# Optimization experiments

Hardware: AMD Instinct MI355X
Metric: run time of the kernel (lower is better)

The kernel has to match this reference:

```python
import jax, jax.numpy as jnp
import numpy as np

# Straight-through sign binarization: forward -> {-1, +1}, backward -> identity
@jax.custom_vjp
def binarize(x):
    return jnp.where(x >= 0, jnp.ones_like(x), -jnp.ones_like(x))

def _bin_fwd(x):
    return binarize(x), None

def _bin_bwd(res, g):
    return (g,)

binarize.defvjp(_bin_fwd, _bin_bwd)

BATCH = 16384
IN_SIZE = 1025   # must be 2**n + 1
HIDDEN = 1025    # must be 2**n + 1

def setup_inputs() -> dict:
    key = jax.random.key(0)
    k0, k1, k2, k3 = jax.random.split(key, 4)
    # weight init scale per reset_parameters: sqrt(1.5/(in+out)) uniform
    s = float(np.sqrt(1.5 / (IN_SIZE + HIDDEN)))
    return {
        "x": jax.random.normal(k0, (BATCH, IN_SIZE), dtype=jnp.float32),
        "W0": jax.random.uniform(k1, (HIDDEN, IN_SIZE), jnp.float32, -s, s),
        "W1": jax.random.uniform(k2, (HIDDEN, HIDDEN), jnp.float32, -s, s),
        "W2": jax.random.uniform(k3, (1, HIDDEN), jnp.float32, -s, s),
    }

def reference(x, W0, W1, W2):
    # x: [B, IN_SIZE]; weights stored [out, in] (nn.Linear convention), no bias
    h = x.reshape(-1, IN_SIZE)
    for W in (W0, W1, W2):
        lin = h @ binarize(W).T          # float GEMM against +/-1 weights
        h = binarize(lin)                # sign activation
    # num_classes == 2 path: to_boolean maps {-1,+1} -> {0,1}, then squeeze
    out = (h + 1.0) * 0.5
    return out.squeeze(-1)               # [B]
```

## Files before the change

### kernel.cpp

```cpp
#include <hip/hip_runtime.h>
#include <cstdint>

typedef unsigned long long u64;
typedef unsigned short ushort_t;
typedef __attribute__((ext_vector_type(8))) short short8;
typedef __attribute__((ext_vector_type(4))) float f32x4;

#define B_TOTAL 16384
#define K_DIM   1025
#define O_DIM   1025
#define NWORDS  17
#define NKT     34
#define NFRAG   72
#define A_BYTES 8192
#define B_BYTES 73728
#define STEP_BYTES (A_BYTES + B_BYTES)
#define FLAG_CAP 4096
#define L23_ROWS 16

__device__ __forceinline__ ushort_t f2bf_rne(float f) {
  unsigned u = __float_as_uint(f);
  return (ushort_t)((u + 0x7fffu + ((u >> 16) & 1u)) >> 16);
}

__device__ __forceinline__ void gload16(const ushort_t* g, char* l) {
  __builtin_amdgcn_global_load_lds(
      (const __attribute__((address_space(1))) void*)g,
      (__attribute__((address_space(3))) void*)l, 16, 0, 0);
}

__global__ __launch_bounds__(256) void pack_all_kernel(const float* __restrict__ W0,
                                                       const float* __restrict__ W1,
                                                       const float* __restrict__ W2,
                                                       u64* __restrict__ w0b,
                                                       u64* __restrict__ w1b,
                                                       u64* __restrict__ w2b) {
  __shared__ unsigned char by[136];
  const int row = blockIdx.x, t = threadIdx.x;
  const float* src; u64* dst; int o;
  if (row < O_DIM)           { src = W0; dst = w0b; o = row; }
  else if (row < 2 * O_DIM)  { src = W1; dst = w1b; o = row - O_DIM; }
  else                       { src = W2; dst = w2b; o = 0; }
  if (t < 136) {
    const float* wr = src + (size_t)o * K_DIM;
    unsigned m = 0;
#pragma unroll
    for (int j = 0; j < 8; ++j) {
      int k = t * 8 + j;
      bool pos = (k < K_DIM) ? (wr[k] >= 0.0f) : true;
      m |= (unsigned)pos << j;
    }
    by[t] = (unsigned char)m;
  }
  __syncthreads();
  if (t < NWORDS) {
    u64 word = 0;
#pragma unroll
    for (int q = 0; q < 8; ++q) word |= (u64)by[t * 8 + q] << (8 * q);
    dst[(size_t)o * NWORDS + t] = word;
  }
}

__global__ __launch_bounds__(256) void prep_sbf_kernel(const float* __restrict__ w0,
                                                       ushort_t* __restrict__ sbf) {
  const int t = threadIdx.x;
  const int f = blockIdx.x * 4 + (t >> 6);
  const int lane = t & 63;
  const int kt = f / NFRAG, nf = f % NFRAG;
  const int o = nf * 16 + (lane & 15);
  const int kbase = kt * 32 + (lane >> 4) * 8;
  short8 sv;
#pragma unroll
  for (int j = 0; j < 8; ++j) {
    int k = kbase + j;
    short v = 0;
    if (o < O_DIM && k < K_DIM)
      v = (short)((w0[(size_t)o * K_DIM + k] >= 0.0f) ? 0x3F80 : 0xBF80);
    sv[j] = v;
  }
  *(short8*)&sbf[(size_t)f * 512 + lane * 8] = sv;
}

__global__ __launch_bounds__(256) void prep_xf_kernel(const float* __restrict__ x,
                                                      ushort_t* __restrict__ xf,
                                                      float* __restrict__ errb) {
  const int p = blockIdx.x, t = threadIdx.x;
  const int mf = t >> 6, lane = t & 63;
  const int lr = lane & 15, lg = lane >> 4;
  const int brow = p * 64 + mf * 16 + lr;
  const float* xr = x + (size_t)brow * K_DIM;
  float s = 0.0f;
  for (int kt = 0; kt < NKT; ++kt) {
    const int kbase = kt * 32 + lg * 8;
    float v[8];
    if (kbase + 8 <= K_DIM) {
      float4 a = *(const float4*)(xr + kbase);
      float4 b = *(const float4*)(xr + kbase + 4);
      v[0]=a.x; v[1]=a.y; v[2]=a.z; v[3]=a.w; v[4]=b.x; v[5]=b.y; v[6]=b.z; v[7]=b.w;
    } else {
#pragma unroll
      for (int j = 0; j < 8; ++j) v[j] = (kbase + j < K_DIM) ? xr[kbase + j] : 0.0f;
    }
    short8 hi, lo;
#pragma unroll
    for (int j = 0; j < 8; ++j) {
      s += fabsf(v[j]);
      ushort_t h = f2bf_rne(v[j]);
      float hf = __uint_as_float((unsigned)h << 16);
      ushort_t l = f2bf_rne(v[j] - hf);
      hi[j] = (short)h; lo[j] = (short)l;
    }
    size_t base = ((size_t)(p * NKT + kt) * 8 + mf) * 512 + lane * 8;
    *(short8*)&xf[base] = hi;
    *(short8*)&xf[base + 4 * 512] = lo;
  }
  s += __shfl_xor(s, 16, 64);
  s += __shfl_xor(s, 32, 64);
  if (lg == 0) errb[brow] = s * (1.02f / 65536.0f) + 0.125f;
}

__global__ __launch_bounds__(512, 2) void l1_fused_kernel(
    const ushort_t* __restrict__ xf, const ushort_t* __restrict__ sbf,
    const float* __restrict__ errb, const float* __restrict__ x,
    const u64* __restrict__ w0b, u64* __restrict__ h1b) {
  extern __shared__ char smem[];
  const int p = blockIdx.x;
  const int t = threadIdx.x;
  const int wave = t >> 6, lane = t & 63;
  const int lr = lane & 15, lg = lane >> 4;
  const int b0 = p * 64;
  const int obase = wave * 144;

  const ushort_t* gA = xf + (size_t)p * NKT * (A_BYTES / 2);

  f32x4 acc[4][9];
#pragma unroll
  for (int mf = 0; mf < 4; ++mf)
#pragma unroll
    for (int nfl = 0; nfl < 9; ++nfl)
#pragma unroll
      for (int c = 0; c < 4; ++c) acc[mf][nfl][c] = 0.0f;

#define STAGE(BUFI, KT)                                                        \
  {                                                                            \
    char* dbuf = smem + (BUFI) * STEP_BYTES;                                   \
    _Pragma("unroll")                                                          \
    for (int i = 0; i < 10; ++i) {                                             \
      int s = wave * 10 + i;                                                   \
      const ushort_t* g = (s < 8)                                              \
          ? gA + (KT) * (A_BYTES / 2) + s * 512 + lane * 8                     \
          : sbf + (size_t)(KT) * (B_BYTES / 2) + (s - 8) * 512 + lane * 8;     \
      gload16(g, dbuf + s * 1024);                                             \
    }                                                                          \
  }

  STAGE(0, 0);
  __syncthreads();
  int cur = 0;
  for (int kt = 0; kt < NKT; ++kt) {
    if (kt + 1 < NKT) STAGE(cur ^ 1, kt + 1);
    const ushort_t* A = (const ushort_t*)(smem + cur * STEP_BYTES);
    const ushort_t* Bf = A + A_BYTES / 2;
    short8 ah[4], al[4];
#pragma unroll
    for (int mf = 0; mf < 4; ++mf) {
      ah[mf] = *(const short8*)&A[mf * 512 + lane * 8];
      al[mf] = *(const short8*)&A[(4 + mf) * 512 + lane * 8];
    }
#pragma unroll
    for (int nfl = 0; nfl < 9; ++nfl) {
      short8 bv = *(const short8*)&Bf[(wave * 9 + nfl) * 512 + lane * 8];
#pragma unroll
      for (int mf = 0; mf < 4; ++mf) {
        acc[mf][nfl] = __builtin_amdgcn_mfma_f32_16x16x32_bf16(ah[mf], bv, acc[mf][nfl], 0, 0, 0);
        acc[mf][nfl] = __builtin_amdgcn_mfma_f32_16x16x32_bf16(al[mf], bv, acc[mf][nfl], 0, 0, 0);
      }
    }
    __syncthreads();
    cur ^= 1;
  }
#undef STAGE

  unsigned char* bits = (unsigned char*)smem;
  u64*      hs   = (u64*)(smem + 73728);
  unsigned* list = (unsigned*)(smem + 82432);
  unsigned* lcnt = (unsigned*)(smem + 98816);
  unsigned* hsw  = (unsigned*)hs;

  if (t == 0) *lcnt = 0;
  __syncthreads();

  float eb[4][4];
#pragma unroll
  for (int mf = 0; mf < 4; ++mf)
#pragma unroll
    for (int rg = 0; rg < 4; ++rg) eb[mf][rg] = errb[b0 + mf * 16 + lg * 4 + rg];

#pragma unroll
  for (int mf = 0; mf < 4; ++mf)
#pragma unroll
    for (int nfl = 0; nfl < 9; ++nfl)
#pragma unroll
      for (int rg = 0; rg < 4; ++rg) {
        int bl = mf * 16 + lg * 4 + rg;
        int o  = obase + nfl * 16 + lr;
        float lin = acc[mf][nfl][rg];
        unsigned abit = (lin >= 0.0f) ? 1u : 0u;
        bits[bl * 1152 + o] = (unsigned char)abit;
        if ((o < O_DIM) && (fabsf(lin) <= eb[mf][rg])) {
          unsigned idx = atomicAdd(lcnt, 1u);
          if (idx < FLAG_CAP)
            list[idx] = ((unsigned)bl << 12) | ((unsigned)o << 1) | abit;
        }
      }
  __syncthreads();

  for (int task = t; task < 64 * NWORDS; task += 512) {
    int row = task / NWORDS, w = task % NWORDS;
    u64 word = 0;
#pragma unroll
    for (int q = 0; q < 8; ++q) {
      u64 v = *(const u64*)&bits[row * 1152 + w * 64 + q * 8];
#pragma unroll
      for (int m = 0; m < 8; ++m)
        word |= ((v >> (8 * m)) & 1ull) << (q * 8 + m);
    }
    int rem = O_DIM - w * 64;
    if (rem < 64) word |= (~0ull << rem);
    hs[row * NWORDS + w] = word;
  }
  __syncthreads();

  {
    unsigned n = *lcnt; if (n > FLAG_CAP) n = FLAG_CAP;
    for (unsigned i = t; i < n; i += 512) {
      unsigned en = list[i];
      int bl = (int)(en >> 12), o = (int)((en >> 1) & 0x7ffu);
      unsigned abit = en & 1u;
      const float* xr = x + (size_t)(b0 + bl) * K_DIM;
      const u64* wr = w0b + (size_t)o * NWORDS;
      float a = 0.0f;
      for (int j = 0; j < 16; ++j) {
        u64 wd = wr[j];
#pragma unroll
        for (int m = 0; m < 64; ++m) {
          float v = xr[j * 64 + m];
          unsigned neg = ((unsigned)(wd >> m) & 1u) ^ 1u;
          a += __uint_as_float(__float_as_uint(v) ^ (neg << 31));
        }
      }
      {
        u64 wd = wr[16];
        float v = xr[1024];
        unsigned neg = ((unsigned)wd & 1u) ^ 1u;
        a += __uint_as_float(__float_as_uint(v) ^ (neg << 31));
      }
      unsigned nb = (a >= 0.0f) ? 1u : 0u;
      if (nb != abit)
        atomicXor(&hsw[bl * 34 + (o >> 5)], 1u << (o & 31));
    }
  }
  __syncthreads();

  for (int task = t; task < 64 * NWORDS; task += 512)
    h1b[(size_t)b0 * NWORDS + task] = hs[task];
}

__global__ __launch_bounds__(256) void l2l3_kernel(const u64* __restrict__ h1b,
                                                   const u64* __restrict__ w1b,
                                                   const u64* __restrict__ w2b,
                                                   float* __restrict__ out) {
  __shared__ u64 hs[L23_ROWS][NWORDS];
  __shared__ u64 h2[L23_ROWS][NWORDS];
  const int bt = blockIdx.x;
  const int t = threadIdx.x;
  for (int i = t; i < L23_ROWS * NWORDS; i += 256)
    hs[i / NWORDS][i % NWORDS] = h1b[(size_t)(bt * L23_ROWS + i / NWORDS) * NWORDS + i % NWORDS];
  __syncthreads();

  const int w = t >> 6, l = t & 63;
  for (int oc = w; oc < NWORDS; oc += 4) {
    int o = oc * 64 + l;
    bool valid = (o < O_DIM);
    int orow = valid ? o : (O_DIM - 1);
    u64 wb[NWORDS];
#pragma unroll
    for (int j = 0; j < NWORDS; ++j) wb[j] = w1b[(size_t)orow * NWORDS + j];
    for (int b = 0; b < L23_ROWS; b += 2) {
      int p0 = 0, p1 = 0;
#pragma unroll
      for (int j = 0; j < NWORDS; ++j) {
        p0 += __popcll(hs[b + 0][j] ^ wb[j]);
        p1 += __popcll(hs[b + 1][j] ^ wb[j]);
      }
      u64 m0 = __ballot(valid ? (K_DIM - 2 * p0 >= 0) : true);
      u64 m1 = __ballot(valid ? (K_DIM - 2 * p1 >= 0) : true);
      if (l == 0) h2[b + 0][oc] = m0;
      if (l == 1) h2[b + 1][oc] = m1;
    }
  }
  __syncthreads();
  if (t < L23_ROWS) {
    int p = 0;
#pragma unroll
    for (int j = 0; j < NWORDS; ++j) p += __popcll(h2[t][j] ^ w2b[j]);
    out[bt * L23_ROWS + t] = ((K_DIM - 2 * p) >= 0) ? 1.0f : 0.0f;
  }
}

extern "C" void kernel_launch(void* const* d_in, const int* in_sizes, int n_in,
                              void* d_out, int out_size, void* d_ws, size_t ws_size,
                              hipStream_t stream) {
  const float* x  = (const float*)d_in[0];
  const float* W0 = (const float*)d_in[1];
  const float* W1 = (const float*)d_in[2];
  const float* W2 = (const float*)d_in[3];
  float* out = (float*)d_out;

  char* ws = (char*)d_ws;
  u64*      w0b  = (u64*)(ws);
  u64*      w1b  = (u64*)(ws + 139776);
  u64*      w2b  = (u64*)(ws + 279552);
  float*    errb = (float*)(ws + 279808);
  u64*      h1b  = (u64*)(ws + 345344);
  ushort_t* sbf  = (ushort_t*)(ws + 2573824);
  ushort_t* xf   = (ushort_t*)(ws + 5080576);

  static bool attr_set = false;
  if (!attr_set) {
    hipFuncSetAttribute((const void*)l1_fused_kernel,
                        hipFuncAttributeMaxDynamicSharedMemorySize, 2 * STEP_BYTES);
    attr_set = true;
  }

  pack_all_kernel<<<2 * O_DIM + 1, 256, 0, stream>>>(W0, W1, W2, w0b, w1b, w2b);
  prep_sbf_kernel<<<NKT * NFRAG / 4, 256, 0, stream>>>(W0, sbf);
  prep_xf_kernel<<<B_TOTAL / 64, 256, 0, stream>>>(x, xf, errb);
  l1_fused_kernel<<<B_TOTAL / 64, 512, 2 * STEP_BYTES, stream>>>(
      xf, sbf, errb, x, w0b, h1b);
  l2l3_kernel<<<B_TOTAL / L23_ROWS, 256, 0, stream>>>(h1b, w1b, w2b, out);
}
```

Baseline: 175.5 us.

## Fuse x bf16 hi/lo split and error-bound computation into layer-1 GEMM kernel

```diff
diff --git a/kernel.cpp b/kernel.cpp
--- a/kernel.cpp
+++ b/kernel.cpp
@@ -81,47 +81,8 @@
   *(short8*)&sbf[(size_t)f * 512 + lane * 8] = sv;
 }
 
-__global__ __launch_bounds__(256) void prep_xf_kernel(const float* __restrict__ x,
-                                                      ushort_t* __restrict__ xf,
-                                                      float* __restrict__ errb) {
-  const int p = blockIdx.x, t = threadIdx.x;
-  const int mf = t >> 6, lane = t & 63;
-  const int lr = lane & 15, lg = lane >> 4;
-  const int brow = p * 64 + mf * 16 + lr;
-  const float* xr = x + (size_t)brow * K_DIM;
-  float s = 0.0f;
-  for (int kt = 0; kt < NKT; ++kt) {
-    const int kbase = kt * 32 + lg * 8;
-    float v[8];
-    if (kbase + 8 <= K_DIM) {
-      float4 a = *(const float4*)(xr + kbase);
-      float4 b = *(const float4*)(xr + kbase + 4);
-      v[0]=a.x; v[1]=a.y; v[2]=a.z; v[3]=a.w; v[4]=b.x; v[5]=b.y; v[6]=b.z; v[7]=b.w;
-    } else {
-#pragma unroll
-      for (int j = 0; j < 8; ++j) v[j] = (kbase + j < K_DIM) ? xr[kbase + j] : 0.0f;
-    }
-    short8 hi, lo;
-#pragma unroll
-    for (int j = 0; j < 8; ++j) {
-      s += fabsf(v[j]);
-      ushort_t h = f2bf_rne(v[j]);
-      float hf = __uint_as_float((unsigned)h << 16);
-      ushort_t l = f2bf_rne(v[j] - hf);
-      hi[j] = (short)h; lo[j] = (short)l;
-    }
-    size_t base = ((size_t)(p * NKT + kt) * 8 + mf) * 512 + lane * 8;
-    *(short8*)&xf[base] = hi;
-    *(short8*)&xf[base + 4 * 512] = lo;
-  }
-  s += __shfl_xor(s, 16, 64);
-  s += __shfl_xor(s, 32, 64);
-  if (lg == 0) errb[brow] = s * (1.02f / 65536.0f) + 0.125f;
-}
-
 __global__ __launch_bounds__(512, 2) void l1_fused_kernel(
-    const ushort_t* __restrict__ xf, const ushort_t* __restrict__ sbf,
-    const float* __restrict__ errb, const float* __restrict__ x,
+    const ushort_t* __restrict__ sbf, const float* __restrict__ x,
     const u64* __restrict__ w0b, u64* __restrict__ h1b) {
   extern __shared__ char smem[];
   const int p = blockIdx.x;
@@ -130,8 +91,9 @@
   const int lr = lane & 15, lg = lane >> 4;
   const int b0 = p * 64;
   const int obase = wave * 144;
-
-  const ushort_t* gA = xf + (size_t)p * NKT * (A_BYTES / 2);
+  const int mf0 = wave;
+
+  const float* xrowA = x + (size_t)(b0 + ((mf0 & 3) * 16 + lr)) * K_DIM;
 
   f32x4 acc[4][9];
 #pragma unroll
@@ -141,24 +103,61 @@
 #pragma unroll
       for (int c = 0; c < 4; ++c) acc[mf][nfl][c] = 0.0f;
 
-#define STAGE(BUFI, KT)                                                        \
+  float xv[8];
+  float sAcc = 0.0f;
+
+#define LOADX(KT)                                                              \
   {                                                                            \
-    char* dbuf = smem + (BUFI) * STEP_BYTES;                                   \
+    int kb = (KT) * 32 + lg * 8;                                               \
+    const float* xr = xrowA + kb;                                              \
+    if (kb + 8 <= K_DIM) {                                                     \
+      float4 a = *(const float4*)xr;                                           \
+      float4 b = *(const float4*)(xr + 4);                                     \
+      xv[0]=a.x; xv[1]=a.y; xv[2]=a.z; xv[3]=a.w;                              \
+      xv[4]=b.x; xv[5]=b.y; xv[6]=b.z; xv[7]=b.w;                              \
+    } else {                                                                   \
+      _Pragma("unroll")                                                        \
+      for (int j = 0; j < 8; ++j) xv[j] = (kb + j < K_DIM) ? xr[j] : 0.0f;     \
+    }                                                                          \
+  }
+
+#define CONVERT_WRITE(DBUF)                                                    \
+  {                                                                            \
+    short8 hi8, lo8;                                                           \
     _Pragma("unroll")                                                          \
-    for (int i = 0; i < 10; ++i) {                                             \
-      int s = wave * 10 + i;                                                   \
-      const ushort_t* g = (s < 8)                                              \
-          ? gA + (KT) * (A_BYTES / 2) + s * 512 + lane * 8                     \
-          : sbf + (size_t)(KT) * (B_BYTES / 2) + (s - 8) * 512 + lane * 8;     \
-      gload16(g, dbuf + s * 1024);                                             \
+    for (int j = 0; j < 8; ++j) {                                              \
+      float v = xv[j];                                                         \
+      sAcc += fabsf(v);                                                        \
+      ushort_t h = f2bf_rne(v);                                                \
+      float hf = __uint_as_float((unsigned)h << 16);                           \
+      ushort_t l2 = f2bf_rne(v - hf);                                          \
+      hi8[j] = (short)h; lo8[j] = (short)l2;                                   \
     }                                                                          \
-  }
-
-  STAGE(0, 0);
-  __syncthreads();
+    *(short8*)((DBUF) + mf0 * 1024 + lane * 16) = hi8;                         \
+    *(short8*)((DBUF) + 4096 + mf0 * 1024 + lane * 16) = lo8;                  \
+  }
+
+#define GLOADB(KT, DBUF)                                                       \
+  {                                                                            \
+    _Pragma("unroll")                                                          \
+    for (int i = 0; i < 9; ++i) {                                              \
+      int sfr = wave * 9 + i;                                                  \
+      gload16(sbf + (size_t)(KT) * (B_BYTES / 2) + sfr * 512 + lane * 8,       \
+              (DBUF) + A_BYTES + sfr * 1024);                                  \
+    }                                                                          \
+  }
+
+  if (t < 256) { LOADX(0); CONVERT_WRITE(smem); }
+  GLOADB(0, smem);
+  __syncthreads();
+
   int cur = 0;
   for (int kt = 0; kt < NKT; ++kt) {
-    if (kt + 1 < NKT) STAGE(cur ^ 1, kt + 1);
+    char* nbuf = smem + (cur ^ 1) * STEP_BYTES;
+    if (kt + 1 < NKT) {
+      if (t < 256) LOADX(kt + 1);
+      GLOADB(kt + 1, nbuf);
+    }
     const ushort_t* A = (const ushort_t*)(smem + cur * STEP_BYTES);
     const ushort_t* Bf = A + A_BYTES / 2;
     short8 ah[4], al[4];
@@ -176,25 +175,33 @@
         acc[mf][nfl] = __builtin_amdgcn_mfma_f32_16x16x32_bf16(al[mf], bv, acc[mf][nfl], 0, 0, 0);
       }
     }
+    if (kt + 1 < NKT && t < 256) CONVERT_WRITE(nbuf);
     __syncthreads();
     cur ^= 1;
   }
-#undef STAGE
+#undef LOADX
+#undef CONVERT_WRITE
+#undef GLOADB
 
   unsigned char* bits = (unsigned char*)smem;
-  u64*      hs   = (u64*)(smem + 73728);
-  unsigned* list = (unsigned*)(smem + 82432);
-  unsigned* lcnt = (unsigned*)(smem + 98816);
-  unsigned* hsw  = (unsigned*)hs;
-
+  u64*      hs    = (u64*)(smem + 73728);
+  unsigned* list  = (unsigned*)(smem + 82432);
+  unsigned* lcnt  = (unsigned*)(smem + 98816);
+  float*    errbL = (float*)(smem + 98832);
+  unsigned* hsw   = (unsigned*)hs;
+
+  sAcc += __shfl_xor(sAcc, 16, 64);
+  sAcc += __shfl_xor(sAcc, 32, 64);
   if (t == 0) *lcnt = 0;
+  if (t < 256 && lg == 0)
+    errbL[mf0 * 16 + lr] = sAcc * (1.02f / 65536.0f) + 0.125f;
   __syncthreads();
 
   float eb[4][4];
 #pragma unroll
   for (int mf = 0; mf < 4; ++mf)
 #pragma unroll
-    for (int rg = 0; rg < 4; ++rg) eb[mf][rg] = errb[b0 + mf * 16 + lg * 4 + rg];
+    for (int rg = 0; rg < 4; ++rg) eb[mf][rg] = errbL[mf * 16 + lg * 4 + rg];
 
 #pragma unroll
   for (int mf = 0; mf < 4; ++mf)
@@ -321,10 +328,8 @@
   u64*      w0b  = (u64*)(ws);
   u64*      w1b  = (u64*)(ws + 139776);
   u64*      w2b  = (u64*)(ws + 279552);
-  float*    errb = (float*)(ws + 279808);
-  u64*      h1b  = (u64*)(ws + 345344);
-  ushort_t* sbf  = (ushort_t*)(ws + 2573824);
-  ushort_t* xf   = (ushort_t*)(ws + 5080576);
+  u64*      h1b  = (u64*)(ws + 280064);
+  ushort_t* sbf  = (ushort_t*)(ws + 2508288);
 
   static bool attr_set = false;
   if (!attr_set) {
@@ -335,8 +340,6 @@
 
   pack_all_kernel<<<2 * O_DIM + 1, 256, 0, stream>>>(W0, W1, W2, w0b, w1b, w2b);
   prep_sbf_kernel<<<NKT * NFRAG / 4, 256, 0, stream>>>(W0, sbf);
-  prep_xf_kernel<<<B_TOTAL / 64, 256, 0, stream>>>(x, xf, errb);
-  l1_fused_kernel<<<B_TOTAL / 64, 512, 2 * STEP_BYTES, stream>>>(
-      xf, sbf, errb, x, w0b, h1b);
+  l1_fused_kernel<<<B_TOTAL / 64, 512, 2 * STEP_BYTES, stream>>>(sbf, x, w0b, h1b);
   l2l3_kernel<<<B_TOTAL / L23_ROWS, 256, 0, stream>>>(h1b, w1b, w2b, out);
 }
```

Measured after the change: 160.4 us. -8.6%, faster.
